# Kernel tuning notes

Measured on AMD Instinct MI355X. Metric: run time of the kernel, lower is better.

## Reference

```python
import jax, jax.numpy as jnp
import numpy as np

NUM_HEADS = 32
WH = WW = 7
DIM = 1024
HEAD_DIM = DIM // NUM_HEADS
SCALE = HEAD_DIM ** -0.5
N = WH * WW
B_ = 1024  # num_windows * batch
NW = 64


def init_relative_position_index(wh):
    # standard Swin relative position index for a square wh x wh window
    coords = np.stack(np.meshgrid(np.arange(wh), np.arange(wh), indexing='ij'))  # 2, wh, wh
    coords = coords.reshape(2, -1)  # 2, N
    rel = coords[:, :, None] - coords[:, None, :]  # 2, N, N
    rel = rel.transpose(1, 2, 0).astype(np.int32)  # N, N, 2
    rel[:, :, 0] += wh - 1
    rel[:, :, 1] += wh - 1
    rel[:, :, 0] *= 2 * wh - 1
    return jnp.asarray(rel.sum(-1), dtype=jnp.int32)  # N, N


def setup_inputs() -> dict:
    key = jax.random.key(0)
    ks = jax.random.split(key, 8)
    x = jax.random.normal(ks[0], (B_, N, DIM), dtype=jnp.float32)
    mask = jax.random.normal(ks[1], (NW, N, N), dtype=jnp.float32)
    qkv_w = jax.random.normal(ks[2], (3 * DIM, DIM), dtype=jnp.float32) * (DIM ** -0.5)
    qkv_b = jax.random.normal(ks[3], (3 * DIM,), dtype=jnp.float32) * 0.02
    rp_bias_table = jax.random.normal(ks[4], ((2 * WH - 1) * (2 * WW - 1), NUM_HEADS), dtype=jnp.float32) * 0.02
    out_w = jax.random.normal(ks[5], (DIM, DIM), dtype=jnp.float32) * (DIM ** -0.5)
    out_b = jax.random.normal(ks[6], (DIM,), dtype=jnp.float32) * 0.02
    rp_index = init_relative_position_index(WH)
    return {"x": x, "mask": mask, "nw": NW, "qkv_w": qkv_w, "qkv_b": qkv_b,
            "rp_bias_table": rp_bias_table, "out_w": out_w, "out_b": out_b,
            "rp_index": rp_index}


def reference(x, mask, nw, qkv_w, qkv_b, rp_bias_table, out_w, out_b, rp_index):
    b_, n, c = x.shape  # (num_windows*B, N, C)
    h, hd = NUM_HEADS, HEAD_DIM
    # QKV projection: (B_, N, 3C)
    qkv = jnp.einsum('bnc,oc->bno', x, qkv_w) + qkv_b
    qkv = qkv.reshape(b_, n, 3, h, hd)
    q = qkv[:, :, 0].transpose(0, 2, 1, 3)  # b h n d
    k = qkv[:, :, 1].transpose(0, 2, 1, 3)
    v = qkv[:, :, 2].transpose(0, 2, 1, 3)
    attn = jnp.einsum('bhnd,bhmd->bhnm', q * SCALE, k)
    # gathered relative position bias: (N, N, H) -> (H, N, N)
    bias = rp_bias_table[rp_index.reshape(-1)].reshape(n, n, h).transpose(2, 0, 1)
    attn = attn + bias[None]
    # add per-window mask: (B, nw, H, N, N)
    attn = attn.reshape(b_ // nw, nw, h, n, n) + mask[None, :, None]
    attn = attn.reshape(b_, h, n, n)
    attn = jax.nn.softmax(attn, axis=-1)
    out = jnp.einsum('bhnm,bhmd->bhnd', attn, v)
    out = out.transpose(0, 2, 1, 3).reshape(b_, n, c)
    out = jnp.einsum('bnc,co->bno', out, out_w) + out_b
    return out
```

## Files before the change

kernel.cpp:

```cpp
#include <hip/hip_runtime.h>
#include <hip/hip_bf16.h>

typedef __bf16 bf16_t;
typedef __bf16 bf16x4 __attribute__((ext_vector_type(4)));
typedef __bf16 bf16x8 __attribute__((ext_vector_type(8)));
typedef float  f32x4  __attribute__((ext_vector_type(4)));

#define NUM_HEADS 32
#define HEAD_DIM 32
#define SEQ 49
#define SEQ2 (SEQ * SEQ)
#define DIM 1024
#define NWIN 64
#define BATCH 1024
#define MTOT (BATCH * SEQ)
#define SCALE 0.17677669529663687f

#define GLOBAL_AS __attribute__((address_space(1)))
#define LDS_AS    __attribute__((address_space(3)))

__device__ __forceinline__ void async_copy16(const bf16_t* g, bf16_t* l)
{
    __builtin_amdgcn_global_load_lds((const GLOBAL_AS uint32_t*)g,
                                     (LDS_AS uint32_t*)l, 16, 0, 0);
}

__global__ __launch_bounds__(256)
void f32_to_bf16(const float* __restrict__ in, bf16_t* __restrict__ out, int n)
{
    int i = (blockIdx.x * 256 + threadIdx.x) * 4;
    if (i < n) {
        float4 v = *(const float4*)(in + i);
        bf16x4 o = { (bf16_t)v.x, (bf16_t)v.y, (bf16_t)v.z, (bf16_t)v.w };
        *(bf16x4*)(out + i) = o;
    }
}

__global__ __launch_bounds__(256)
void transpose1024(const float* __restrict__ in, bf16_t* __restrict__ out)
{
    __shared__ float tile[32][33];
    const int bx = blockIdx.x, by = blockIdx.y;
    const int tx = threadIdx.x & 31, ty = threadIdx.x >> 5;
    for (int r = ty; r < 32; r += 8)
        tile[r][tx] = in[(size_t)(by * 32 + r) * 1024 + bx * 32 + tx];
    __syncthreads();
    for (int r = ty; r < 32; r += 8)
        out[(size_t)(bx * 32 + r) * 1024 + by * 32 + tx] = (bf16_t)tile[tx][r];
}

__global__ __launch_bounds__(256)
void bias_gather_t(const float* __restrict__ rp_table, const int* __restrict__ rp_index,
                   float* __restrict__ biasT)
{
    int idx = blockIdx.x * 256 + threadIdx.x;
    if (idx < NUM_HEADS * SEQ2) {
        int h   = idx / SEQ2;
        int rem = idx - h * SEQ2;
        int j = rem / SEQ, i = rem - j * SEQ;
        biasT[idx] = rp_table[rp_index[i * SEQ + j] * NUM_HEADS + h];
    }
}

__global__ __launch_bounds__(256)
void mask_transpose(const float* __restrict__ mask, float* __restrict__ maskT)
{
    int idx = blockIdx.x * 256 + threadIdx.x;
    if (idx < NWIN * SEQ2) {
        int wd  = idx / SEQ2;
        int rem = idx - wd * SEQ2;
        int j = rem / SEQ, i = rem - j * SEQ;
        maskT[idx] = mask[wd * SEQ2 + i * SEQ + j];
    }
}

template<typename TC>
__global__ __launch_bounds__(256)
void gemm_bt(const bf16_t* __restrict__ A, int lda,
             const bf16_t* __restrict__ W,
             const float* __restrict__ bias,
             TC* __restrict__ C, int N, int K)
{
    __shared__ __align__(16) bf16_t As[128][32];
    __shared__ __align__(16) bf16_t Ws[128][32];

    const int tid  = threadIdx.x;
    const int lane = tid & 63;
    const int wave = tid >> 6;
    const int wm = wave >> 1, wn = wave & 1;
    const int l15 = lane & 15, lqq = lane >> 4;
    const int m0 = blockIdx.y * 128;
    const int n0 = blockIdx.x * 128;

    f32x4 acc[4][4] = {};

    for (int k0 = 0; k0 < K; k0 += 32) {
        #pragma unroll
        for (int it = 0; it < 2; ++it) {
            int c   = it * 256 + wave * 64 + lane;
            int row = c >> 2;
            int col = (c & 3) << 3;
            bf16_t* lbA = &As[0][0] + (size_t)(it * 256 + wave * 64) * 8;
            bf16_t* lbW = &Ws[0][0] + (size_t)(it * 256 + wave * 64) * 8;
            async_copy16(A + (size_t)(m0 + row) * lda + k0 + col, lbA);
            async_copy16(W + (size_t)(n0 + row) * K   + k0 + col, lbW);
        }
        __syncthreads();

        bf16x8 af[4], wf[4];
        #pragma unroll
        for (int i = 0; i < 4; ++i)
            af[i] = *(const bf16x8*)(&As[wm * 64 + i * 16 + l15][lqq * 8]);
        #pragma unroll
        for (int j = 0; j < 4; ++j)
            wf[j] = *(const bf16x8*)(&Ws[wn * 64 + j * 16 + l15][lqq * 8]);

        #pragma unroll
        for (int i = 0; i < 4; ++i)
            #pragma unroll
            for (int j = 0; j < 4; ++j)
                acc[i][j] = __builtin_amdgcn_mfma_f32_16x16x32_bf16(
                    af[i], wf[j], acc[i][j], 0, 0, 0);
        __syncthreads();
    }

    #pragma unroll
    for (int i = 0; i < 4; ++i) {
        #pragma unroll
        for (int j = 0; j < 4; ++j) {
            int col = n0 + wn * 64 + j * 16 + l15;
            float bv = bias[col];
            #pragma unroll
            for (int r = 0; r < 4; ++r) {
                int row = m0 + wm * 64 + i * 16 + lqq * 4 + r;
                C[(size_t)row * N + col] = (TC)(acc[i][j][r] + bv);
            }
        }
    }
}

__global__ __launch_bounds__(256, 4)
void attn_mfma(bf16_t* __restrict__ qkv, const float* __restrict__ maskT,
               const float* __restrict__ biasT)
{
    __shared__ __align__(16) bf16_t qs[64][40];
    __shared__ __align__(16) bf16_t ks[64][40];
    __shared__ __align__(16) bf16_t vt[32][72];
    __shared__ __align__(16) bf16_t Ps[64][72];

    const int tid  = threadIdx.x;
    const int lane = tid & 63;
    const int wv   = tid >> 6;
    const int l15  = lane & 15, lq = lane >> 4;
    const int b  = blockIdx.x >> 5;
    const int h  = blockIdx.x & 31;
    const int wd = b & (NWIN - 1);
    const size_t base = (size_t)b * (SEQ * 3 * DIM) + h * HEAD_DIM;

    {
        const int n  = tid >> 2;
        const int c8 = (tid & 3) << 3;
        const bf16_t* g = qkv + base + (size_t)n * (3 * DIM);
        *(uint4*)(&qs[n][c8]) = *(const uint4*)(g + c8);
        *(uint4*)(&ks[n][c8]) = *(const uint4*)(g + DIM + c8);
        uint4 v = *(const uint4*)(g + 2 * DIM + c8);
        const bf16_t* pv = (const bf16_t*)&v;
        #pragma unroll
        for (int j = 0; j < 8; ++j) vt[c8 + j][n] = pv[j];
    }
    __syncthreads();

    const f32x4 zero4 = {0.f, 0.f, 0.f, 0.f};
    const int iq = wv * 16 + l15;
    bf16x8 qf = *(const bf16x8*)(&qs[iq][lq * 8]);
    f32x4 sacc[4];
    #pragma unroll
    for (int jt = 0; jt < 4; ++jt) {
        bf16x8 kf = *(const bf16x8*)(&ks[jt * 16 + l15][lq * 8]);
        sacc[jt] = __builtin_amdgcn_mfma_f32_16x16x32_bf16(kf, qf, zero4, 0, 0, 0);
    }

    const bool iv = iq < SEQ;
    const float* bT = biasT + (size_t)h  * SEQ2 + iq;
    const float* mT = maskT + (size_t)wd * SEQ2 + iq;
    float p[16];
    #pragma unroll
    for (int jt = 0; jt < 4; ++jt)
        #pragma unroll
        for (int r = 0; r < 4; ++r) {
            int j = jt * 16 + lq * 4 + r;
            float v = -1e30f;
            if (iv && j < SEQ)
                v = sacc[jt][r] * SCALE + bT[j * SEQ] + mT[j * SEQ];
            p[jt * 4 + r] = v;
        }

    float m = p[0];
    #pragma unroll
    for (int t = 1; t < 16; ++t) m = fmaxf(m, p[t]);
    m = fmaxf(m, __shfl_xor(m, 16));
    m = fmaxf(m, __shfl_xor(m, 32));
    float sum = 0.f;
    #pragma unroll
    for (int t = 0; t < 16; ++t) { p[t] = __expf(p[t] - m); sum += p[t]; }
    sum += __shfl_xor(sum, 16);
    sum += __shfl_xor(sum, 32);
    const float inv = 1.f / sum;

    #pragma unroll
    for (int jt = 0; jt < 4; ++jt) {
        bf16x4 q4 = { (bf16_t)(p[jt * 4 + 0] * inv), (bf16_t)(p[jt * 4 + 1] * inv),
                      (bf16_t)(p[jt * 4 + 2] * inv), (bf16_t)(p[jt * 4 + 3] * inv) };
        *(bf16x4*)(&Ps[iq][jt * 16 + lq * 4]) = q4;
    }
    __syncthreads();

    bf16x8 pf0 = *(const bf16x8*)(&Ps[iq][lq * 8]);
    bf16x8 pf1 = *(const bf16x8*)(&Ps[iq][32 + lq * 8]);
    #pragma unroll
    for (int dt = 0; dt < 2; ++dt) {
        bf16x8 vf0 = *(const bf16x8*)(&vt[dt * 16 + l15][lq * 8]);
        bf16x8 vf1 = *(const bf16x8*)(&vt[dt * 16 + l15][32 + lq * 8]);
        f32x4 o = __builtin_amdgcn_mfma_f32_16x16x32_bf16(pf0, vf0, zero4, 0, 0, 0);
        o = __builtin_amdgcn_mfma_f32_16x16x32_bf16(pf1, vf1, o, 0, 0, 0);
        #pragma unroll
        for (int r = 0; r < 4; ++r) {
            int i = wv * 16 + lq * 4 + r;
            if (i < SEQ)
                qkv[base + (size_t)i * (3 * DIM) + dt * 16 + l15] = (bf16_t)o[r];
        }
    }
}

extern "C" void kernel_launch(void* const* d_in, const int* in_sizes, int n_in,
                              void* d_out, int out_size, void* d_ws, size_t ws_size,
                              hipStream_t stream)
{
    const float* x        = (const float*)d_in[0];
    const float* mask     = (const float*)d_in[1];
    const float* qkv_w    = (const float*)d_in[3];
    const float* qkv_b    = (const float*)d_in[4];
    const float* rp_table = (const float*)d_in[5];
    const float* out_w    = (const float*)d_in[6];
    const float* out_b    = (const float*)d_in[7];
    const int*   rp_index = (const int*)d_in[8];
    float* out = (float*)d_out;

    bf16_t* qkv = (bf16_t*)d_ws;
    bf16_t* wT  = (bf16_t*)((char*)d_ws + (size_t)MTOT * 3072 * sizeof(bf16_t));

    bf16_t* xb    = (bf16_t*)d_out;
    bf16_t* wb    = (bf16_t*)((char*)d_out + (size_t)MTOT * DIM * sizeof(bf16_t));
    float*  biasT = (float*)((char*)d_out + (size_t)MTOT * DIM * sizeof(bf16_t)
                                          + (size_t)3 * DIM * DIM * sizeof(bf16_t));
    float*  maskT = biasT + (size_t)NUM_HEADS * SEQ2;

    f32_to_bf16<<<(MTOT * DIM / 4 + 255) / 256, 256, 0, stream>>>(x, xb, MTOT * DIM);
    f32_to_bf16<<<(3 * DIM * DIM / 4 + 255) / 256, 256, 0, stream>>>(qkv_w, wb, 3 * DIM * DIM);
    transpose1024<<<dim3(32, 32), 256, 0, stream>>>(out_w, wT);
    bias_gather_t<<<(NUM_HEADS * SEQ2 + 255) / 256, 256, 0, stream>>>(rp_table, rp_index, biasT);
    mask_transpose<<<(NWIN * SEQ2 + 255) / 256, 256, 0, stream>>>(mask, maskT);

    gemm_bt<bf16_t><<<dim3(3072 / 128, MTOT / 128), 256, 0, stream>>>(
        xb, DIM, wb, qkv_b, qkv, 3072, DIM);

    attn_mfma<<<dim3(BATCH * NUM_HEADS), 256, 0, stream>>>(qkv, maskT, biasT);

    gemm_bt<float><<<dim3(1024 / 128, MTOT / 128), 256, 0, stream>>>(
        qkv, 3072, wT, out_b, out, DIM, DIM);
}
```

Measured before the change: 1.169 ms.

## Replace GEMM with 256x256 double-buffered, XOR-swizzled LDS MFMA kernel

```diff
diff --git a/kernel.cpp b/kernel.cpp
--- a/kernel.cpp
+++ b/kernel.cpp
@@ -74,69 +74,123 @@
     }
 }
 
+#define READ_A(MH)                                                        \
+    { _Pragma("unroll")                                                   \
+      for (int m_ = 0; m_ < 4; ++m_) {                                    \
+        _Pragma("unroll")                                                 \
+        for (int ks_ = 0; ks_ < 2; ++ks_) {                               \
+            int row_ = wr * 128 + (MH) * 64 + m_ * 16 + l15;              \
+            af[m_][ks_] = *(const bf16x8*)(Ab + row_ * 64 +               \
+                          (((ks_ * 4 + lq) ^ (row_ & 7)) << 3));          \
+        } } }
+
+#define READ_B(BF, NH)                                                    \
+    { _Pragma("unroll")                                                   \
+      for (int n_ = 0; n_ < 2; ++n_) {                                    \
+        _Pragma("unroll")                                                 \
+        for (int ks_ = 0; ks_ < 2; ++ks_) {                               \
+            int row_ = wc * 64 + (NH) * 32 + n_ * 16 + l15;               \
+            BF[n_][ks_] = *(const bf16x8*)(Bb + row_ * 64 +               \
+                          (((ks_ * 4 + lq) ^ (row_ & 7)) << 3));          \
+        } } }
+
+#define MFMA_Q(MH, NH, BF)                                                \
+    { __builtin_amdgcn_s_setprio(1);                                      \
+      _Pragma("unroll")                                                   \
+      for (int m_ = 0; m_ < 4; ++m_) {                                    \
+        _Pragma("unroll")                                                 \
+        for (int n_ = 0; n_ < 2; ++n_) {                                  \
+            acc[(MH) * 4 + m_][(NH) * 2 + n_] =                           \
+                __builtin_amdgcn_mfma_f32_16x16x32_bf16(af[m_][0], BF[n_][0], \
+                    acc[(MH) * 4 + m_][(NH) * 2 + n_], 0, 0, 0);          \
+            acc[(MH) * 4 + m_][(NH) * 2 + n_] =                           \
+                __builtin_amdgcn_mfma_f32_16x16x32_bf16(af[m_][1], BF[n_][1], \
+                    acc[(MH) * 4 + m_][(NH) * 2 + n_], 0, 0, 0);          \
+        } }                                                               \
+      __builtin_amdgcn_s_setprio(0); }
+
+#define STAGE_KTILE(DA, DB, K0)                                           \
+    { _Pragma("unroll")                                                   \
+      for (int r_ = 0; r_ < 4; ++r_) {                                    \
+        int s_   = r_ * 512 + tid;                                        \
+        int row_ = s_ >> 3;                                               \
+        int col_ = ((s_ & 7) ^ (row_ & 7)) << 3;                          \
+        async_copy16(A + (size_t)(m0 + row_) * lda + (K0) + col_,         \
+                     (DA) + ((r_ * 512 + (wave << 6)) << 3));             \
+        async_copy16(W + (size_t)(n0 + row_) * ldw + (K0) + col_,         \
+                     (DB) + ((r_ * 512 + (wave << 6)) << 3));             \
+      } }
+
 template<typename TC>
-__global__ __launch_bounds__(256)
-void gemm_bt(const bf16_t* __restrict__ A, int lda,
-             const bf16_t* __restrict__ W,
+__global__ __launch_bounds__(512, 2)
+void gemm256(const bf16_t* __restrict__ A, int lda,
+             const bf16_t* __restrict__ W, int ldw,
              const float* __restrict__ bias,
              TC* __restrict__ C, int N, int K)
 {
-    __shared__ __align__(16) bf16_t As[128][32];
-    __shared__ __align__(16) bf16_t Ws[128][32];
+    __shared__ __align__(16) bf16_t Abuf[2][256 * 64];
+    __shared__ __align__(16) bf16_t Bbuf[2][256 * 64];
 
     const int tid  = threadIdx.x;
     const int lane = tid & 63;
     const int wave = tid >> 6;
-    const int wm = wave >> 1, wn = wave & 1;
-    const int l15 = lane & 15, lqq = lane >> 4;
-    const int m0 = blockIdx.y * 128;
-    const int n0 = blockIdx.x * 128;
-
-    f32x4 acc[4][4] = {};
-
-    for (int k0 = 0; k0 < K; k0 += 32) {
+    const int wr = wave >> 2;
+    const int wc = wave & 3;
+    const int l15 = lane & 15, lq = lane >> 4;
+    const int m0 = blockIdx.y * 256;
+    const int n0 = blockIdx.x * 256;
+    const int nkt = K >> 6;
+
+    f32x4 acc[8][4] = {};
+    bf16x8 af[4][2], bf0[2][2], bf1[2][2];
+
+    STAGE_KTILE(Abuf[0], Bbuf[0], 0);
+    asm volatile("s_waitcnt vmcnt(0)" ::: "memory");
+    __syncthreads();
+
+    for (int t = 0; t < nkt; ++t) {
+        const bf16_t* Ab = Abuf[t & 1];
+        const bf16_t* Bb = Bbuf[t & 1];
+
+        if (t + 1 < nkt)
+            STAGE_KTILE(Abuf[(t + 1) & 1], Bbuf[(t + 1) & 1], (t + 1) << 6);
+        READ_A(0);
+        READ_B(bf0, 0);
+        __builtin_amdgcn_s_barrier();
+        MFMA_Q(0, 0, bf0);
+        __builtin_amdgcn_s_barrier();
+        READ_B(bf1, 1);
+        __builtin_amdgcn_s_barrier();
+        MFMA_Q(0, 1, bf1);
+        __builtin_amdgcn_s_barrier();
+        READ_A(1);
+        __builtin_amdgcn_s_barrier();
+        MFMA_Q(1, 1, bf1);
+        __builtin_amdgcn_s_barrier();
+        READ_B(bf0, 0);
+        __builtin_amdgcn_s_barrier();
+        MFMA_Q(1, 0, bf0);
+        asm volatile("s_waitcnt vmcnt(0)" ::: "memory");
+        __builtin_amdgcn_s_barrier();
+        __builtin_amdgcn_sched_barrier(0);
+    }
+
+    #pragma unroll
+    for (int mh = 0; mh < 2; ++mh)
+      #pragma unroll
+      for (int m = 0; m < 4; ++m)
         #pragma unroll
-        for (int it = 0; it < 2; ++it) {
-            int c   = it * 256 + wave * 64 + lane;
-            int row = c >> 2;
-            int col = (c & 3) << 3;
-            bf16_t* lbA = &As[0][0] + (size_t)(it * 256 + wave * 64) * 8;
-            bf16_t* lbW = &Ws[0][0] + (size_t)(it * 256 + wave * 64) * 8;
-            async_copy16(A + (size_t)(m0 + row) * lda + k0 + col, lbA);
-            async_copy16(W + (size_t)(n0 + row) * K   + k0 + col, lbW);
-        }
-        __syncthreads();
-
-        bf16x8 af[4], wf[4];
-        #pragma unroll
-        for (int i = 0; i < 4; ++i)
-            af[i] = *(const bf16x8*)(&As[wm * 64 + i * 16 + l15][lqq * 8]);
-        #pragma unroll
-        for (int j = 0; j < 4; ++j)
-            wf[j] = *(const bf16x8*)(&Ws[wn * 64 + j * 16 + l15][lqq * 8]);
-
-        #pragma unroll
-        for (int i = 0; i < 4; ++i)
-            #pragma unroll
-            for (int j = 0; j < 4; ++j)
-                acc[i][j] = __builtin_amdgcn_mfma_f32_16x16x32_bf16(
-                    af[i], wf[j], acc[i][j], 0, 0, 0);
-        __syncthreads();
-    }
-
-    #pragma unroll
-    for (int i = 0; i < 4; ++i) {
-        #pragma unroll
-        for (int j = 0; j < 4; ++j) {
-            int col = n0 + wn * 64 + j * 16 + l15;
-            float bv = bias[col];
+        for (int nh = 0; nh < 2; ++nh)
+          #pragma unroll
+          for (int n = 0; n < 2; ++n) {
+            const int col = n0 + wc * 64 + nh * 32 + n * 16 + l15;
+            const float bv = bias[col];
             #pragma unroll
             for (int r = 0; r < 4; ++r) {
-                int row = m0 + wm * 64 + i * 16 + lqq * 4 + r;
-                C[(size_t)row * N + col] = (TC)(acc[i][j][r] + bv);
+                const int row = m0 + wr * 128 + mh * 64 + m * 16 + lq * 4 + r;
+                C[(size_t)row * N + col] = (TC)(acc[mh * 4 + m][nh * 2 + n][r] + bv);
             }
-        }
-    }
+          }
 }
 
 __global__ __launch_bounds__(256, 4)
@@ -261,11 +315,11 @@
     bias_gather_t<<<(NUM_HEADS * SEQ2 + 255) / 256, 256, 0, stream>>>(rp_table, rp_index, biasT);
     mask_transpose<<<(NWIN * SEQ2 + 255) / 256, 256, 0, stream>>>(mask, maskT);
 
-    gemm_bt<bf16_t><<<dim3(3072 / 128, MTOT / 128), 256, 0, stream>>>(
-        xb, DIM, wb, qkv_b, qkv, 3072, DIM);
+    gemm256<bf16_t><<<dim3(3072 / 256, MTOT / 256), 512, 0, stream>>>(
+        xb, DIM, wb, DIM, qkv_b, qkv, 3072, DIM);
 
     attn_mfma<<<dim3(BATCH * NUM_HEADS), 256, 0, stream>>>(qkv, maskT, biasT);
 
-    gemm_bt<float><<<dim3(1024 / 128, MTOT / 128), 256, 0, stream>>>(
-        qkv, 3072, wT, out_b, out, DIM, DIM);
-}
+    gemm256<float><<<dim3(1024 / 256, MTOT / 256), 512, 0, stream>>>(
+        qkv, 3072, wT, DIM, out_b, out, DIM, DIM);
+}
```

Measured after the change: 1.206 ms. 1.03x slower.
